# Kernel optimization log

Hardware: AMD Instinct MI355X
Metric: run time of the kernel (lower is better)

## Reference

```python
import jax, jax.numpy as jnp
import numpy as np

SHIFT_HZ = 20.0
SAMPLE_RATE = 16000
N_FFT = 512
SHIFT_BINS = SHIFT_HZ / (SAMPLE_RATE / N_FFT)  # 0.64 bins
EPS = 1e-08


def setup_inputs() -> dict:
    key = jax.random.key(0)
    # log-magnitude spectrogram [B, 1, F, T]
    x = jax.random.normal(key, (32, 1, 257, 4096), dtype=jnp.float32)
    return {"x": x}


def reference(x):
    B, C, F, T = x.shape
    x_lin = jnp.power(10.0, x[:, 0])  # [B, F, T] linear magnitude

    f = jnp.arange(F, dtype=jnp.float32)
    target = f + SHIFT_BINS                     # source bin (fractional)
    f_low = jnp.floor(target)
    f_high = jnp.ceil(target)
    alpha = (target - f_low).astype(x.dtype)    # interp weight; 0 when integer

    valid = (target >= 0) & (target < F) & (f_low < F) & (f_high < F)
    lo = jnp.clip(f_low.astype(jnp.int32), 0, F - 1)
    hi = jnp.clip(f_high.astype(jnp.int32), 0, F - 1)

    # gather along frequency axis + linear interp (alpha==0 reduces to copy)
    interp = ((1.0 - alpha)[None, :, None] * jnp.take(x_lin, lo, axis=1)
              + alpha[None, :, None] * jnp.take(x_lin, hi, axis=1))
    shifted = jnp.where(valid[None, :, None], interp, 0.0)

    return jnp.log10(shifted + EPS)[:, None]    # [B, 1, F, T]
```

## Files before the change

### kernel.cpp

```cpp
#include <hip/hip_runtime.h>

#define B_DIM 32
#define F_DIM 257
#define T_DIM 4096
#define EPS_F 1e-8f

#define LOG2_10  3.32192809488736234787f
#define LOG10_2  0.30102999566398119521f

__device__ __forceinline__ float pow10_fast(float v) {
    return __builtin_amdgcn_exp2f(v * LOG2_10);
}

__device__ __forceinline__ float log10_fast(float v) {
    return __builtin_amdgcn_logf(v) * LOG10_2;
}

__global__ __launch_bounds__(256) void freq_shift_kernel(
        const float* __restrict__ x, float* __restrict__ out) {
    const int bf = blockIdx.x;
    const int f  = bf % F_DIM;
    const long long base = (long long)bf * T_DIM;
    const int tid = threadIdx.x;

    float4* __restrict__ orow = (float4*)(out + base);

    if (f == F_DIM - 1) {
        const float cv = log10_fast(EPS_F);
        const float4 v = make_float4(cv, cv, cv, cv);
#pragma unroll
        for (int i = 0; i < T_DIM / 4 / 256; ++i)
            orow[i * 256 + tid] = v;
        return;
    }

    const float4* __restrict__ row0 = (const float4*)(x + base);
    const float4* __restrict__ row1 = (const float4*)(x + base + T_DIM);

    const float ff     = (float)f;
    const float target = ff + 0.64f;
    const float alpha  = target - ff;
    const float beta   = 1.0f - alpha;

#pragma unroll
    for (int i = 0; i < T_DIM / 4 / 256; ++i) {
        const int j = i * 256 + tid;
        const float4 a = row0[j];
        const float4 b = row1[j];
        float4 r;
        r.x = log10_fast(beta * pow10_fast(a.x) + alpha * pow10_fast(b.x) + EPS_F);
        r.y = log10_fast(beta * pow10_fast(a.y) + alpha * pow10_fast(b.y) + EPS_F);
        r.z = log10_fast(beta * pow10_fast(a.z) + alpha * pow10_fast(b.z) + EPS_F);
        r.w = log10_fast(beta * pow10_fast(a.w) + alpha * pow10_fast(b.w) + EPS_F);
        orow[j] = r;
    }
}

extern "C" void kernel_launch(void* const* d_in, const int* in_sizes, int n_in,
                              void* d_out, int out_size, void* d_ws, size_t ws_size,
                              hipStream_t stream) {
    const float* x = (const float*)d_in[0];
    float* out = (float*)d_out;
    dim3 grid(B_DIM * F_DIM);
    dim3 block(256);
    freq_shift_kernel<<<grid, block, 0, stream>>>(x, out);
}
```

Measured before the change: 225.0 us.

## Process strips of frequency rows per thread to reuse loaded rows

Each thread now handles 8 consecutive frequency rows for one float4 column. It loads 9 input rows and computes pow10 once per row, so each row is shared by neighbouring outputs. Before, every output row reloaded two input rows and recomputed both exponentials, which roughly doubled global reads and exp work. The grid becomes 3D (column group, strip, batch), with a separate strip that writes the constant last row. The cost is more registers per thread and fewer threads in flight.

```diff
diff --git a/kernel.cpp b/kernel.cpp
--- a/kernel.cpp
+++ b/kernel.cpp
@@ -3,6 +3,8 @@
 #define B_DIM 32
 #define F_DIM 257
 #define T_DIM 4096
+#define TV    (T_DIM / 4)
+#define R     8
 #define EPS_F 1e-8f
 
 #define LOG2_10  3.32192809488736234787f
@@ -11,48 +13,50 @@
 __device__ __forceinline__ float pow10_fast(float v) {
     return __builtin_amdgcn_exp2f(v * LOG2_10);
 }
-
 __device__ __forceinline__ float log10_fast(float v) {
     return __builtin_amdgcn_logf(v) * LOG10_2;
 }
 
-__global__ __launch_bounds__(256) void freq_shift_kernel(
+__global__ __launch_bounds__(256) void freq_shift_strip(
         const float* __restrict__ x, float* __restrict__ out) {
-    const int bf = blockIdx.x;
-    const int f  = bf % F_DIM;
-    const long long base = (long long)bf * T_DIM;
-    const int tid = threadIdx.x;
+    const int cg  = blockIdx.x;
+    const int s   = blockIdx.y;
+    const int b   = blockIdx.z;
+    const int col = cg * 256 + threadIdx.x;
 
-    float4* __restrict__ orow = (float4*)(out + base);
+    const long long bbase = (long long)b * F_DIM * T_DIM;
+    float4* __restrict__ orow = (float4*)(out + bbase);
 
-    if (f == F_DIM - 1) {
+    if (s == 32) {
         const float cv = log10_fast(EPS_F);
-        const float4 v = make_float4(cv, cv, cv, cv);
-#pragma unroll
-        for (int i = 0; i < T_DIM / 4 / 256; ++i)
-            orow[i * 256 + tid] = v;
+        orow[(F_DIM - 1) * TV + col] = make_float4(cv, cv, cv, cv);
         return;
     }
 
-    const float4* __restrict__ row0 = (const float4*)(x + base);
-    const float4* __restrict__ row1 = (const float4*)(x + base + T_DIM);
+    const int f0 = s * R;
+    const float4* __restrict__ xrow = (const float4*)(x + bbase);
 
-    const float ff     = (float)f;
-    const float target = ff + 0.64f;
-    const float alpha  = target - ff;
-    const float beta   = 1.0f - alpha;
+    float4 e[R + 1];
+#pragma unroll
+    for (int k = 0; k <= R; ++k) {
+        const float4 a = xrow[(f0 + k) * TV + col];
+        e[k].x = pow10_fast(a.x);
+        e[k].y = pow10_fast(a.y);
+        e[k].z = pow10_fast(a.z);
+        e[k].w = pow10_fast(a.w);
+    }
 
 #pragma unroll
-    for (int i = 0; i < T_DIM / 4 / 256; ++i) {
-        const int j = i * 256 + tid;
-        const float4 a = row0[j];
-        const float4 b = row1[j];
-        float4 r;
-        r.x = log10_fast(beta * pow10_fast(a.x) + alpha * pow10_fast(b.x) + EPS_F);
-        r.y = log10_fast(beta * pow10_fast(a.y) + alpha * pow10_fast(b.y) + EPS_F);
-        r.z = log10_fast(beta * pow10_fast(a.z) + alpha * pow10_fast(b.z) + EPS_F);
-        r.w = log10_fast(beta * pow10_fast(a.w) + alpha * pow10_fast(b.w) + EPS_F);
-        orow[j] = r;
+    for (int r = 0; r < R; ++r) {
+        const float ff    = (float)(f0 + r);
+        const float alpha = (ff + 0.64f) - ff;
+        const float beta  = 1.0f - alpha;
+        float4 o;
+        o.x = log10_fast(beta * e[r].x + alpha * e[r + 1].x + EPS_F);
+        o.y = log10_fast(beta * e[r].y + alpha * e[r + 1].y + EPS_F);
+        o.z = log10_fast(beta * e[r].z + alpha * e[r + 1].z + EPS_F);
+        o.w = log10_fast(beta * e[r].w + alpha * e[r + 1].w + EPS_F);
+        orow[(f0 + r) * TV + col] = o;
     }
 }
 
@@ -61,7 +65,7 @@
                               hipStream_t stream) {
     const float* x = (const float*)d_in[0];
     float* out = (float*)d_out;
-    dim3 grid(B_DIM * F_DIM);
+    dim3 grid(T_DIM / 4 / 256, F_DIM / R + 1, B_DIM);
     dim3 block(256);
-    freq_shift_kernel<<<grid, block, 0, stream>>>(x, out);
+    freq_shift_strip<<<grid, block, 0, stream>>>(x, out);
 }
```

Result: slower. 231.5 us (+2.9%).
